# Optimization experiments

Measured on AMD Instinct MI355X. Metric: run time of the kernel, lower is better.

Reference implementation:

```python
import jax, jax.numpy as jnp
import numpy as np

M = 64          # SOM grid rows
N_GRID = 64     # SOM grid cols
DIM = 768       # SapBERT hidden size
COMPS = M * N_GRID
NBATCH = 8192   # number of embedded vectors per step


def setup_inputs() -> dict:
    key = jax.random.key(0)
    k1, k2 = jax.random.split(key)
    embedded = jax.random.normal(k1, (NBATCH, DIM), dtype=jnp.float32)
    contents = jax.random.normal(k2, (M, N_GRID, DIM), dtype=jnp.float32)
    # grid_dists: squared pairwise distances between grid coordinates (pdist2 in init_grid)
    x, y = np.meshgrid(range(M), range(N_GRID))
    g = np.stack([x, y]).reshape(2, -1).astype(np.float32)  # [2, comps]
    sq = (g ** 2).sum(0)
    gd = sq[:, None] + sq[None, :] - 2.0 * (g.T @ g)
    grid_dists = jnp.asarray(gd, dtype=jnp.float32)
    sigma = jnp.float32(max(M, N_GRID) / 2.0)
    return {"embedded": embedded, "contents": contents,
            "grid_dists": grid_dists, "sigma": sigma}


def reference(embedded, contents, grid_dists, sigma):
    comps = grid_dists.shape[0]
    dim = embedded.shape[1]
    flat_c = contents.reshape(comps, dim)
    # Gaussian neighborhood weights (compute_weight, weighted=True)
    weights = jnp.exp(-grid_dists / (2.0 * sigma ** 2))  # [comps, comps]
    # find_bmu: squared L2 dist + argmin (expanded form, same argmin as
    # the materialized N x comps x dim diff tensor in the original)
    dist = ((embedded ** 2).sum(-1, keepdims=True)
            + (flat_c ** 2).sum(-1)[None, :]
            - 2.0 * embedded @ flat_c.T)                 # [N, comps]
    min_idx = jnp.argmin(dist, axis=1)                   # [N]
    # scatter-accumulate counts and sums per codebook entry (index_add_)
    freq = jnp.zeros((comps,), embedded.dtype).at[min_idx].add(1.0)
    sums = jnp.zeros((comps, dim), embedded.dtype).at[min_idx].add(embedded)
    used = freq > 0
    avg = jnp.where(used[:, None], sums / jnp.maximum(freq, 1.0)[:, None], flat_c)
    # freq_weights[i,j] = weights[i,j] * freq[i]; update_num = sum_j fw[i,j]*avg[j,d]
    num = freq[:, None] * (weights @ avg)                # [comps, dim]
    denom = freq * weights.sum(axis=1)                   # [comps]
    update = num / jnp.where(used, denom, 1.0)[:, None]
    new_flat = jnp.where(used[:, None], update, flat_c)  # only update_denom!=0 rows
    new_contents = new_flat.reshape(contents.shape)
    delta = jnp.linalg.norm(new_contents - contents, axis=-1).sum()
    return delta, new_contents
```

## Files before the change

### kernel.cpp

```cpp
#include <hip/hip_runtime.h>

#define NB 8192
#define COMPS 4096
#define DIM 768

typedef _Float16 half8_t __attribute__((ext_vector_type(8)));
typedef float floatx4 __attribute__((ext_vector_type(4)));
typedef unsigned short ushort4_t __attribute__((ext_vector_type(4)));
typedef unsigned short ushort8_t __attribute__((ext_vector_type(8)));
typedef unsigned long long ullx2 __attribute__((ext_vector_type(2)));

typedef __attribute__((address_space(1))) const void* gas_ptr;
typedef __attribute__((address_space(3))) void* las_ptr;

__device__ __forceinline__ void gl_lds16(const _Float16* g, _Float16* l) {
  __builtin_amdgcn_global_load_lds((gas_ptr)(const void*)g, (las_ptr)(void*)l, 16, 0, 0);
}

__device__ __forceinline__ unsigned long long pack_min(float v, int col) {
  unsigned u = __float_as_uint(v);
  u = (u & 0x80000000u) ? ~u : (u | 0x80000000u);
  return ((unsigned long long)u << 32) | (unsigned)col;
}

#define PREP_GRID 13401
__global__ void k_prep(const float* __restrict__ e, const float* __restrict__ c,
                       const float* __restrict__ sigma,
                       _Float16* __restrict__ ehi, _Float16* __restrict__ elo,
                       _Float16* __restrict__ chi, _Float16* __restrict__ clo,
                       float* __restrict__ cnorm, float* __restrict__ E,
                       float* __restrict__ rE, float* __restrict__ sums,
                       float* __restrict__ freq, float* __restrict__ rowsq,
                       unsigned long long* __restrict__ packed,
                       unsigned int* __restrict__ done) {
  int bx = blockIdx.x, t = threadIdx.x;
  if (bx < 6144) {
    int id = bx * 256 + t;
    float4 v = ((const float4*)e)[id];
    ushort4_t h, l;
    float xs[4] = {v.x, v.y, v.z, v.w};
#pragma unroll
    for (int q = 0; q < 4; ++q) {
      _Float16 hh = (_Float16)xs[q];
      _Float16 ll = (_Float16)(xs[q] - (float)hh);
      h[q] = __builtin_bit_cast(unsigned short, hh);
      l[q] = __builtin_bit_cast(unsigned short, ll);
    }
    ((ushort4_t*)ehi)[id] = h;
    ((ushort4_t*)elo)[id] = l;
  } else if (bx < 10240) {
    int i = bx - 6144;
    float s = 0.f;
    if (t < 192) {
      float4 v = ((const float4*)c)[i * 192 + t];
      float xs[4] = {v.x, v.y, v.z, v.w};
      ushort4_t h, l;
#pragma unroll
      for (int q = 0; q < 4; ++q) {
        _Float16 hh = (_Float16)xs[q];
        _Float16 ll = (_Float16)(xs[q] - (float)hh);
        h[q] = __builtin_bit_cast(unsigned short, hh);
        l[q] = __builtin_bit_cast(unsigned short, ll);
        s = fmaf(xs[q], xs[q], s);
      }
      ((ushort4_t*)chi)[i * 192 + t] = h;
      ((ushort4_t*)clo)[i * 192 + t] = l;
    }
#pragma unroll
    for (int o = 32; o; o >>= 1) s += __shfl_down(s, o);
    __shared__ float red[3];
    if (t < 192 && (t & 63) == 0) red[t >> 6] = s;
    __syncthreads();
    if (t == 0) cnorm[i] = red[0] + red[1] + red[2];
  } else if (bx < 10304) {
    int i = bx - 10240;
    if (t < 64) {
      float sg = sigma[0];
      float inv = -1.0f / (2.0f * sg * sg);
      float d = (float)(i - t);
      float v = expf(d * d * inv);
      E[i * 64 + t] = v;
      float s = v;
#pragma unroll
      for (int o = 32; o; o >>= 1) s += __shfl_down(s, o);
      if (t == 0) rE[i] = s;
    }
  } else if (bx < 13376) {
    int id = (bx - 10304) * 256 + t;
    floatx4 z = {0.f, 0.f, 0.f, 0.f};
    ((floatx4*)sums)[id] = z;
  } else if (bx < 13392) {
    int id = (bx - 13376) * 256 + t;
    ullx2 f = {~0ULL, ~0ULL};
    ((ullx2*)packed)[id] = f;
  } else if (bx < 13396) {
    int id = (bx - 13392) * 256 + t;
    floatx4 z = {0.f, 0.f, 0.f, 0.f};
    ((floatx4*)freq)[id] = z;
  } else if (bx < 13400) {
    int id = (bx - 13396) * 256 + t;
    floatx4 z = {0.f, 0.f, 0.f, 0.f};
    ((floatx4*)rowsq)[id] = z;
  } else {
    if (t == 0) *done = 0u;
  }
}

__launch_bounds__(256)
__global__ void k_gemm1(const _Float16* __restrict__ ehi, const _Float16* __restrict__ elo,
                        const _Float16* __restrict__ chi, const _Float16* __restrict__ clo,
                        const float* __restrict__ cnorm,
                        unsigned long long* __restrict__ packed) {
  __shared__ _Float16 Ah[128 * 64], Al[128 * 64], Bh[128 * 64], Bl[128 * 64];
  int tid = threadIdx.x;
  int lane = tid & 63, w = tid >> 6;
  int wr = w >> 1, wc = w & 1;
  int g = lane >> 4, rl = lane & 15;
  int i0 = blockIdx.x * 128, j0 = blockIdx.y * 128;

  int lr = lane >> 3, lc = lane & 7;
  int cch = lc ^ lr;
  const _Float16* gsrc;
  _Float16* dbuf;
  if (w == 0)      { gsrc = ehi + (size_t)i0 * DIM; dbuf = Ah; }
  else if (w == 1) { gsrc = elo + (size_t)i0 * DIM; dbuf = Al; }
  else if (w == 2) { gsrc = chi + (size_t)j0 * DIM; dbuf = Bh; }
  else             { gsrc = clo + (size_t)j0 * DIM; dbuf = Bl; }
  gsrc += (size_t)lr * DIM + cch * 8;
  _Float16* dst = dbuf + lane * 8;

  floatx4 acc[4][4] = {};

  for (int kt = 0; kt < DIM; kt += 64) {
    __syncthreads();
#pragma unroll
    for (int q = 0; q < 16; ++q)
      gl_lds16(gsrc + kt + (size_t)(q * 8) * DIM, dst + q * 512);
    __syncthreads();

#pragma unroll
    for (int s = 0; s < 2; ++s) {
      half8_t ah[4], al[4];
#pragma unroll
      for (int m = 0; m < 4; ++m) {
        int r = wr * 64 + m * 16 + rl;
        int p = (s * 4 + g) ^ (rl & 7);
        ah[m] = *(half8_t*)&Ah[r * 64 + p * 8];
        al[m] = *(half8_t*)&Al[r * 64 + p * 8];
      }
#pragma unroll
      for (int n = 0; n < 4; ++n) {
        int r = wc * 64 + n * 16 + rl;
        int p = (s * 4 + g) ^ (rl & 7);
        half8_t bh = *(half8_t*)&Bh[r * 64 + p * 8];
        half8_t bl = *(half8_t*)&Bl[r * 64 + p * 8];
#pragma unroll
        for (int m = 0; m < 4; ++m) {
          acc[m][n] = __builtin_amdgcn_mfma_f32_16x16x32_f16(ah[m], bh, acc[m][n], 0, 0, 0);
          acc[m][n] = __builtin_amdgcn_mfma_f32_16x16x32_f16(ah[m], bl, acc[m][n], 0, 0, 0);
          acc[m][n] = __builtin_amdgcn_mfma_f32_16x16x32_f16(al[m], bh, acc[m][n], 0, 0, 0);
        }
      }
    }
  }

  float cn[4];
#pragma unroll
  for (int n = 0; n < 4; ++n) cn[n] = cnorm[j0 + wc * 64 + n * 16 + rl];

#pragma unroll
  for (int m = 0; m < 4; ++m) {
#pragma unroll
    for (int j = 0; j < 4; ++j) {
      int row = i0 + wr * 64 + m * 16 + g * 4 + j;
      float best = 3.0e38f;
      int bcol = 0;
#pragma unroll
      for (int n = 0; n < 4; ++n) {
        float d = fmaf(-2.0f, acc[m][n][j], cn[n]);
        int col = j0 + wc * 64 + n * 16 + rl;
        if (d < best) { best = d; bcol = col; }
      }
      unsigned long long pk = pack_min(best, bcol);
#pragma unroll
      for (int o = 1; o < 16; o <<= 1) {
        unsigned long long other = __shfl_xor(pk, o);
        if (other < pk) pk = other;
      }
      if (rl == 0) atomicMin(&packed[row], pk);
    }
  }
}

__global__ void k_scatter(const float* __restrict__ e,
                          const unsigned long long* __restrict__ packed,
                          float* __restrict__ freq, float* __restrict__ sums) {
  int i = blockIdx.x, t = threadIdx.x;
  int idx = (int)(packed[i] & 0xffffffffULL);
  if (t == 0) unsafeAtomicAdd(&freq[idx], 1.0f);
#pragma unroll
  for (int r = 0; r < 3; ++r) {
    int d = t + 256 * r;
    unsafeAtomicAdd(&sums[(size_t)idx * DIM + d], e[(size_t)i * DIM + d]);
  }
}

__global__ void k_t1(const float* __restrict__ sums, const float* __restrict__ freq,
                     const float* __restrict__ cont, const float* __restrict__ E,
                     float* __restrict__ T1) {
  __shared__ float S[64 * 128];
  __shared__ float Esh[64 * 64];
  int a = blockIdx.x, db = blockIdx.y, t = threadIdx.x;
#pragma unroll
  for (int it = 0; it < 8; ++it) {
    int id = t + 256 * it;
    int row = id >> 5, c4 = id & 31;
    int comp = a * 64 + row;
    float f = freq[comp];
    size_t o = (size_t)comp * 192 + db * 32 + c4;
    floatx4 v;
    if (f > 0.f) {
      floatx4 sv = ((const floatx4*)sums)[o];
      float inv = 1.0f / f;
      v = sv * inv;
    } else v = ((const floatx4*)cont)[o];
    ((floatx4*)S)[id] = v;
  }
#pragma unroll
  for (int it = 0; it < 4; ++it) {
    int id = t + 256 * it;
    ((floatx4*)Esh)[id] = ((const floatx4*)E)[id];
  }
  __syncthreads();

  int d4 = t & 31, b0 = (t >> 5) * 8;
  floatx4 acc[8] = {};
  for (int bp = 0; bp < 64; ++bp) {
    floatx4 sv = ((floatx4*)S)[bp * 32 + d4];
#pragma unroll
    for (int b = 0; b < 8; ++b)
      acc[b] += Esh[(b0 + b) * 64 + bp] * sv;
  }
#pragma unroll
  for (int b = 0; b < 8; ++b)
    ((floatx4*)T1)[(size_t)(a * 64 + b0 + b) * 192 + db * 32 + d4] = acc[b];
}

__global__ void k_wnum(const float* __restrict__ T1, const float* __restrict__ E,
                       const float* __restrict__ rE, const float* __restrict__ freq,
                       const float* __restrict__ cont, float* __restrict__ out,
                       float* __restrict__ rowsq, unsigned int* __restrict__ done) {
  __shared__ float S[64 * 128];
  __shared__ float Esh[64 * 64];
  int b = blockIdx.x, db = blockIdx.y, t = threadIdx.x;
#pragma unroll
  for (int it = 0; it < 8; ++it) {
    int id = t + 256 * it;
    int ap = id >> 5, c4 = id & 31;
    ((floatx4*)S)[id] = ((const floatx4*)T1)[(size_t)(ap * 64 + b) * 192 + db * 32 + c4];
  }
#pragma unroll
  for (int it = 0; it < 4; ++it) {
    int id = t + 256 * it;
    ((floatx4*)Esh)[id] = ((const floatx4*)E)[id];
  }
  __syncthreads();

  int d4 = t & 31, a0 = (t >> 5) * 8;
  floatx4 acc[8] = {};
  for (int ap = 0; ap < 64; ++ap) {
    floatx4 tv = ((floatx4*)S)[ap * 32 + d4];
#pragma unroll
    for (int a = 0; a < 8; ++a)
      acc[a] += Esh[(a0 + a) * 64 + ap] * tv;
  }

  float rb = rE[b];
  float sq[8];
#pragma unroll
  for (int a = 0; a < 8; ++a) {
    int comp = (a0 + a) * 64 + b;
    bool used = freq[comp] > 0.f;
    floatx4 cv = ((const floatx4*)cont)[(size_t)comp * 192 + db * 32 + d4];
    floatx4 val;
    if (used) {
      float inv = 1.0f / (rE[a0 + a] * rb);
      val = acc[a] * inv;
    } else val = cv;
    size_t base = 1 + (size_t)comp * DIM + db * 128 + d4 * 4;
    out[base] = val[0]; out[base + 1] = val[1];
    out[base + 2] = val[2]; out[base + 3] = val[3];
    floatx4 df = val - cv;
    sq[a] = df[0] * df[0] + df[1] * df[1] + df[2] * df[2] + df[3] * df[3];
  }
#pragma unroll
  for (int a = 0; a < 8; ++a) {
#pragma unroll
    for (int o = 1; o < 32; o <<= 1) sq[a] += __shfl_xor(sq[a], o);
  }
  if (d4 == 0) {
#pragma unroll
    for (int a = 0; a < 8; ++a)
      unsafeAtomicAdd(&rowsq[(a0 + a) * 64 + b], sq[a]);
  }

  __shared__ unsigned int lastflag;
  __syncthreads();
  if (t == 0) {
    __threadfence();
    unsigned int old = atomicAdd(done, 1u);
    lastflag = (old == 64u * 6u - 1u) ? 1u : 0u;
  }
  __syncthreads();
  if (lastflag) {
    double s = 0.0;
    for (int c2 = t; c2 < COMPS; c2 += 256) {
      float r = __hip_atomic_load(&rowsq[c2], __ATOMIC_RELAXED,
                                  __HIP_MEMORY_SCOPE_AGENT);
      s += sqrt((double)r);
    }
#pragma unroll
    for (int o = 32; o; o >>= 1) s += __shfl_down(s, o);
    __shared__ double red[4];
    if ((t & 63) == 0) red[t >> 6] = s;
    __syncthreads();
    if (t == 0) out[0] = (float)(red[0] + red[1] + red[2] + red[3]);
  }
}

extern "C" void kernel_launch(void* const* d_in, const int* in_sizes, int n_in,
                              void* d_out, int out_size, void* d_ws, size_t ws_size,
                              hipStream_t stream) {
  const float* e = (const float*)d_in[0];
  const float* cont = (const float*)d_in[1];
  const float* sigma = (const float*)d_in[3];
  float* out = (float*)d_out;

  char* ws = (char*)d_ws;
  size_t off = 0;
  auto take = [&](size_t bytes) { char* p = ws + off; off += (bytes + 255) & ~(size_t)255; return p; };

  unsigned long long* packed = (unsigned long long*)take(NB * 8);
  float* freq  = (float*)take(COMPS * 4);
  float* rowsq = (float*)take(COMPS * 4);
  float* cnorm = (float*)take(COMPS * 4);
  float* E     = (float*)take(64 * 64 * 4);
  float* rE    = (float*)take(64 * 4);
  unsigned int* done = (unsigned int*)take(256);
  float* sums  = (float*)take((size_t)COMPS * DIM * 4);
  char* U = take((size_t)NB * DIM * 2 * 2 + (size_t)COMPS * DIM * 2 * 2);
  _Float16* ehi = (_Float16*)U;
  _Float16* elo = (_Float16*)(U + (size_t)NB * DIM * 2);
  _Float16* chi = (_Float16*)(U + (size_t)NB * DIM * 4);
  _Float16* clo = (_Float16*)(U + (size_t)NB * DIM * 4 + (size_t)COMPS * DIM * 2);
  float* T1 = (float*)(U + (size_t)NB * DIM * 4);

  k_prep<<<PREP_GRID, 256, 0, stream>>>(e, cont, sigma, ehi, elo, chi, clo,
                                        cnorm, E, rE, sums, freq, rowsq,
                                        packed, done);
  k_gemm1<<<dim3(NB / 128, COMPS / 128), 256, 0, stream>>>(ehi, elo, chi, clo, cnorm, packed);
  k_scatter<<<NB, 256, 0, stream>>>(e, packed, freq, sums);
  k_t1<<<dim3(64, 6), 256, 0, stream>>>(sums, freq, cont, E, T1);
  k_wnum<<<dim3(64, 6), 256, 0, stream>>>(T1, E, rE, freq, cont, out, rowsq, done);
}
```

Before: 345.6 us.

## Double-buffer GEMM LDS tiles and fuse tail kernels with grid barriers

The distance GEMM now uses a K-step of 32 and two LDS buffers, so the global-to-LDS loads for the next tile are issued while the current tile is being multiplied. This replaces the earlier single-buffered 64-wide tile that stalled on a full sync before each compute step, and it drops the XOR swizzle. The scatter, T1 and wnum kernels are merged into one persistent 384-block kernel separated by software grid barriers, which removes two kernel launches. The grid barriers rely on all 384 blocks being resident at once, and dropping the swizzle may cause LDS bank conflicts.

```diff
diff --git a/kernel.cpp b/kernel.cpp
--- a/kernel.cpp
+++ b/kernel.cpp
@@ -3,11 +3,11 @@
 #define NB 8192
 #define COMPS 4096
 #define DIM 768
+#define TAIL_BLOCKS 384
 
 typedef _Float16 half8_t __attribute__((ext_vector_type(8)));
 typedef float floatx4 __attribute__((ext_vector_type(4)));
 typedef unsigned short ushort4_t __attribute__((ext_vector_type(4)));
-typedef unsigned short ushort8_t __attribute__((ext_vector_type(8)));
 typedef unsigned long long ullx2 __attribute__((ext_vector_type(2)));
 
 typedef __attribute__((address_space(1))) const void* gas_ptr;
@@ -32,7 +32,7 @@
                        float* __restrict__ rE, float* __restrict__ sums,
                        float* __restrict__ freq, float* __restrict__ rowsq,
                        unsigned long long* __restrict__ packed,
-                       unsigned int* __restrict__ done) {
+                       unsigned int* __restrict__ tk) {
   int bx = blockIdx.x, t = threadIdx.x;
   if (bx < 6144) {
     int id = bx * 256 + t;
@@ -102,7 +102,7 @@
     floatx4 z = {0.f, 0.f, 0.f, 0.f};
     ((floatx4*)rowsq)[id] = z;
   } else {
-    if (t == 0) *done = 0u;
+    if (t < 64) tk[t] = 0u;
   }
 }
 
@@ -111,57 +111,65 @@
                         const _Float16* __restrict__ chi, const _Float16* __restrict__ clo,
                         const float* __restrict__ cnorm,
                         unsigned long long* __restrict__ packed) {
-  __shared__ _Float16 Ah[128 * 64], Al[128 * 64], Bh[128 * 64], Bl[128 * 64];
+  __shared__ _Float16 lds[2][4][128 * 32];
   int tid = threadIdx.x;
   int lane = tid & 63, w = tid >> 6;
   int wr = w >> 1, wc = w & 1;
   int g = lane >> 4, rl = lane & 15;
   int i0 = blockIdx.x * 128, j0 = blockIdx.y * 128;
 
-  int lr = lane >> 3, lc = lane & 7;
-  int cch = lc ^ lr;
+  int lr = lane >> 2, lc = lane & 3;
   const _Float16* gsrc;
-  _Float16* dbuf;
-  if (w == 0)      { gsrc = ehi + (size_t)i0 * DIM; dbuf = Ah; }
-  else if (w == 1) { gsrc = elo + (size_t)i0 * DIM; dbuf = Al; }
-  else if (w == 2) { gsrc = chi + (size_t)j0 * DIM; dbuf = Bh; }
-  else             { gsrc = clo + (size_t)j0 * DIM; dbuf = Bl; }
-  gsrc += (size_t)lr * DIM + cch * 8;
-  _Float16* dst = dbuf + lane * 8;
+  if (w == 0)      gsrc = ehi + (size_t)i0 * DIM;
+  else if (w == 1) gsrc = elo + (size_t)i0 * DIM;
+  else if (w == 2) gsrc = chi + (size_t)j0 * DIM;
+  else             gsrc = clo + (size_t)j0 * DIM;
+  gsrc += (size_t)lr * DIM + lc * 8;
 
   floatx4 acc[4][4] = {};
 
-  for (int kt = 0; kt < DIM; kt += 64) {
-    __syncthreads();
-#pragma unroll
-    for (int q = 0; q < 16; ++q)
-      gl_lds16(gsrc + kt + (size_t)(q * 8) * DIM, dst + q * 512);
-    __syncthreads();
-
-#pragma unroll
-    for (int s = 0; s < 2; ++s) {
-      half8_t ah[4], al[4];
+  {
+    _Float16* dst = &lds[0][w][0] + lane * 8;
+#pragma unroll
+    for (int q = 0; q < 8; ++q)
+      gl_lds16(gsrc + (size_t)(q * 16) * DIM, dst + q * 512);
+  }
+  __syncthreads();
+
+  const int NT = DIM / 32;
+  for (int t = 0; t < NT; ++t) {
+    int cur = t & 1;
+    if (t + 1 < NT) {
+      const _Float16* gs = gsrc + (t + 1) * 32;
+      _Float16* dst = &lds[cur ^ 1][w][0] + lane * 8;
+#pragma unroll
+      for (int q = 0; q < 8; ++q)
+        gl_lds16(gs + (size_t)(q * 16) * DIM, dst + q * 512);
+    }
+    const _Float16* Ah = lds[cur][0];
+    const _Float16* Al = lds[cur][1];
+    const _Float16* Bh = lds[cur][2];
+    const _Float16* Bl = lds[cur][3];
+    half8_t ah[4], al[4];
+#pragma unroll
+    for (int m = 0; m < 4; ++m) {
+      int off = (wr * 64 + m * 16 + rl) * 32 + g * 8;
+      ah[m] = *(const half8_t*)&Ah[off];
+      al[m] = *(const half8_t*)&Al[off];
+    }
+#pragma unroll
+    for (int n = 0; n < 4; ++n) {
+      int off = (wc * 64 + n * 16 + rl) * 32 + g * 8;
+      half8_t bh = *(const half8_t*)&Bh[off];
+      half8_t bl = *(const half8_t*)&Bl[off];
 #pragma unroll
       for (int m = 0; m < 4; ++m) {
-        int r = wr * 64 + m * 16 + rl;
-        int p = (s * 4 + g) ^ (rl & 7);
-        ah[m] = *(half8_t*)&Ah[r * 64 + p * 8];
-        al[m] = *(half8_t*)&Al[r * 64 + p * 8];
-      }
-#pragma unroll
-      for (int n = 0; n < 4; ++n) {
-        int r = wc * 64 + n * 16 + rl;
-        int p = (s * 4 + g) ^ (rl & 7);
-        half8_t bh = *(half8_t*)&Bh[r * 64 + p * 8];
-        half8_t bl = *(half8_t*)&Bl[r * 64 + p * 8];
-#pragma unroll
-        for (int m = 0; m < 4; ++m) {
-          acc[m][n] = __builtin_amdgcn_mfma_f32_16x16x32_f16(ah[m], bh, acc[m][n], 0, 0, 0);
-          acc[m][n] = __builtin_amdgcn_mfma_f32_16x16x32_f16(ah[m], bl, acc[m][n], 0, 0, 0);
-          acc[m][n] = __builtin_amdgcn_mfma_f32_16x16x32_f16(al[m], bh, acc[m][n], 0, 0, 0);
-        }
-      }
-    }
+        acc[m][n] = __builtin_amdgcn_mfma_f32_16x16x32_f16(ah[m], bh, acc[m][n], 0, 0, 0);
+        acc[m][n] = __builtin_amdgcn_mfma_f32_16x16x32_f16(ah[m], bl, acc[m][n], 0, 0, 0);
+        acc[m][n] = __builtin_amdgcn_mfma_f32_16x16x32_f16(al[m], bh, acc[m][n], 0, 0, 0);
+      }
+    }
+    __syncthreads();
   }
 
   float cn[4];
@@ -192,139 +200,152 @@
   }
 }
 
-__global__ void k_scatter(const float* __restrict__ e,
-                          const unsigned long long* __restrict__ packed,
-                          float* __restrict__ freq, float* __restrict__ sums) {
-  int i = blockIdx.x, t = threadIdx.x;
-  int idx = (int)(packed[i] & 0xffffffffULL);
-  if (t == 0) unsafeAtomicAdd(&freq[idx], 1.0f);
-#pragma unroll
-  for (int r = 0; r < 3; ++r) {
-    int d = t + 256 * r;
-    unsafeAtomicAdd(&sums[(size_t)idx * DIM + d], e[(size_t)i * DIM + d]);
-  }
-}
-
-__global__ void k_t1(const float* __restrict__ sums, const float* __restrict__ freq,
-                     const float* __restrict__ cont, const float* __restrict__ E,
-                     float* __restrict__ T1) {
+__device__ __forceinline__ void gbar(unsigned int* tk) {
+  __syncthreads();
+  if (threadIdx.x == 0) {
+    __hip_atomic_fetch_add(tk, 1u, __ATOMIC_RELEASE, __HIP_MEMORY_SCOPE_AGENT);
+    while (__hip_atomic_load(tk, __ATOMIC_ACQUIRE, __HIP_MEMORY_SCOPE_AGENT)
+           < (unsigned)TAIL_BLOCKS) {
+      __builtin_amdgcn_s_sleep(8);
+    }
+  }
+  __syncthreads();
+}
+
+__launch_bounds__(256, 2)
+__global__ void k_tail(const float* __restrict__ e,
+                       const unsigned long long* __restrict__ packed,
+                       const float* __restrict__ cont, const float* __restrict__ E,
+                       const float* __restrict__ rE,
+                       float* __restrict__ freq, float* __restrict__ sums,
+                       float* __restrict__ T1, float* __restrict__ rowsq,
+                       float* __restrict__ out, unsigned int* __restrict__ tk) {
   __shared__ float S[64 * 128];
   __shared__ float Esh[64 * 64];
-  int a = blockIdx.x, db = blockIdx.y, t = threadIdx.x;
-#pragma unroll
-  for (int it = 0; it < 8; ++it) {
-    int id = t + 256 * it;
-    int row = id >> 5, c4 = id & 31;
-    int comp = a * 64 + row;
-    float f = freq[comp];
-    size_t o = (size_t)comp * 192 + db * 32 + c4;
-    floatx4 v;
-    if (f > 0.f) {
-      floatx4 sv = ((const floatx4*)sums)[o];
-      float inv = 1.0f / f;
-      v = sv * inv;
-    } else v = ((const floatx4*)cont)[o];
-    ((floatx4*)S)[id] = v;
+  int bid = blockIdx.x, t = threadIdx.x;
+
+  for (int i = bid; i < NB; i += TAIL_BLOCKS) {
+    int idx = (int)(packed[i] & 0xffffffffULL);
+    if (t == 0) unsafeAtomicAdd(&freq[idx], 1.0f);
+#pragma unroll
+    for (int r = 0; r < 3; ++r) {
+      int d = t + 256 * r;
+      unsafeAtomicAdd(&sums[(size_t)idx * DIM + d], e[(size_t)i * DIM + d]);
+    }
   }
 #pragma unroll
   for (int it = 0; it < 4; ++it) {
     int id = t + 256 * it;
     ((floatx4*)Esh)[id] = ((const floatx4*)E)[id];
   }
-  __syncthreads();
-
-  int d4 = t & 31, b0 = (t >> 5) * 8;
-  floatx4 acc[8] = {};
-  for (int bp = 0; bp < 64; ++bp) {
-    floatx4 sv = ((floatx4*)S)[bp * 32 + d4];
-#pragma unroll
-    for (int b = 0; b < 8; ++b)
-      acc[b] += Esh[(b0 + b) * 64 + bp] * sv;
-  }
-#pragma unroll
-  for (int b = 0; b < 8; ++b)
-    ((floatx4*)T1)[(size_t)(a * 64 + b0 + b) * 192 + db * 32 + d4] = acc[b];
-}
-
-__global__ void k_wnum(const float* __restrict__ T1, const float* __restrict__ E,
-                       const float* __restrict__ rE, const float* __restrict__ freq,
-                       const float* __restrict__ cont, float* __restrict__ out,
-                       float* __restrict__ rowsq, unsigned int* __restrict__ done) {
-  __shared__ float S[64 * 128];
-  __shared__ float Esh[64 * 64];
-  int b = blockIdx.x, db = blockIdx.y, t = threadIdx.x;
-#pragma unroll
-  for (int it = 0; it < 8; ++it) {
-    int id = t + 256 * it;
-    int ap = id >> 5, c4 = id & 31;
-    ((floatx4*)S)[id] = ((const floatx4*)T1)[(size_t)(ap * 64 + b) * 192 + db * 32 + c4];
-  }
-#pragma unroll
-  for (int it = 0; it < 4; ++it) {
-    int id = t + 256 * it;
-    ((floatx4*)Esh)[id] = ((const floatx4*)E)[id];
-  }
-  __syncthreads();
-
-  int d4 = t & 31, a0 = (t >> 5) * 8;
-  floatx4 acc[8] = {};
-  for (int ap = 0; ap < 64; ++ap) {
-    floatx4 tv = ((floatx4*)S)[ap * 32 + d4];
-#pragma unroll
-    for (int a = 0; a < 8; ++a)
-      acc[a] += Esh[(a0 + a) * 64 + ap] * tv;
-  }
-
-  float rb = rE[b];
-  float sq[8];
-#pragma unroll
-  for (int a = 0; a < 8; ++a) {
-    int comp = (a0 + a) * 64 + b;
-    bool used = freq[comp] > 0.f;
-    floatx4 cv = ((const floatx4*)cont)[(size_t)comp * 192 + db * 32 + d4];
-    floatx4 val;
-    if (used) {
-      float inv = 1.0f / (rE[a0 + a] * rb);
-      val = acc[a] * inv;
-    } else val = cv;
-    size_t base = 1 + (size_t)comp * DIM + db * 128 + d4 * 4;
-    out[base] = val[0]; out[base + 1] = val[1];
-    out[base + 2] = val[2]; out[base + 3] = val[3];
-    floatx4 df = val - cv;
-    sq[a] = df[0] * df[0] + df[1] * df[1] + df[2] * df[2] + df[3] * df[3];
-  }
-#pragma unroll
-  for (int a = 0; a < 8; ++a) {
-#pragma unroll
-    for (int o = 1; o < 32; o <<= 1) sq[a] += __shfl_xor(sq[a], o);
-  }
-  if (d4 == 0) {
-#pragma unroll
-    for (int a = 0; a < 8; ++a)
-      unsafeAtomicAdd(&rowsq[(a0 + a) * 64 + b], sq[a]);
-  }
-
-  __shared__ unsigned int lastflag;
-  __syncthreads();
-  if (t == 0) {
-    __threadfence();
-    unsigned int old = atomicAdd(done, 1u);
-    lastflag = (old == 64u * 6u - 1u) ? 1u : 0u;
-  }
-  __syncthreads();
-  if (lastflag) {
-    double s = 0.0;
-    for (int c2 = t; c2 < COMPS; c2 += 256) {
-      float r = __hip_atomic_load(&rowsq[c2], __ATOMIC_RELAXED,
-                                  __HIP_MEMORY_SCOPE_AGENT);
-      s += sqrt((double)r);
-    }
-#pragma unroll
-    for (int o = 32; o; o >>= 1) s += __shfl_down(s, o);
-    __shared__ double red[4];
-    if ((t & 63) == 0) red[t >> 6] = s;
-    __syncthreads();
-    if (t == 0) out[0] = (float)(red[0] + red[1] + red[2] + red[3]);
+  gbar(&tk[0]);
+
+  {
+    int a = bid / 6, db = bid % 6;
+#pragma unroll
+    for (int it = 0; it < 8; ++it) {
+      int id = t + 256 * it;
+      int row = id >> 5, c4 = id & 31;
+      int comp = a * 64 + row;
+      float f = freq[comp];
+      size_t o = (size_t)comp * 192 + db * 32 + c4;
+      floatx4 v;
+      if (f > 0.f) {
+        floatx4 sv = ((const floatx4*)sums)[o];
+        v = sv * (1.0f / f);
+      } else v = ((const floatx4*)cont)[o];
+      ((floatx4*)S)[id] = v;
+    }
+    __syncthreads();
+
+    int d4 = t & 31, b0 = (t >> 5) * 8;
+    floatx4 acc[8] = {};
+    for (int bp = 0; bp < 64; ++bp) {
+      floatx4 sv = ((floatx4*)S)[bp * 32 + d4];
+#pragma unroll
+      for (int b = 0; b < 8; ++b)
+        acc[b] += Esh[(b0 + b) * 64 + bp] * sv;
+    }
+#pragma unroll
+    for (int b = 0; b < 8; ++b) {
+      size_t base = ((size_t)(a * 64 + b0 + b) * 192 + db * 32 + d4) * 4;
+#pragma unroll
+      for (int q = 0; q < 4; ++q)
+        __hip_atomic_store(&T1[base + q], acc[b][q], __ATOMIC_RELAXED,
+                           __HIP_MEMORY_SCOPE_AGENT);
+    }
+  }
+  gbar(&tk[1]);
+
+  {
+    int b = bid / 6, db = bid % 6;
+#pragma unroll
+    for (int it = 0; it < 8; ++it) {
+      int id = t + 256 * it;
+      int ap = id >> 5, c4 = id & 31;
+      ((floatx4*)S)[id] =
+          ((const floatx4*)T1)[(size_t)(ap * 64 + b) * 192 + db * 32 + c4];
+    }
+    __syncthreads();
+
+    int d4 = t & 31, a0 = (t >> 5) * 8;
+    floatx4 acc[8] = {};
+    for (int ap = 0; ap < 64; ++ap) {
+      floatx4 tv = ((floatx4*)S)[ap * 32 + d4];
+#pragma unroll
+      for (int a = 0; a < 8; ++a)
+        acc[a] += Esh[(a0 + a) * 64 + ap] * tv;
+    }
+
+    float rb = rE[b];
+    float sq[8];
+#pragma unroll
+    for (int a = 0; a < 8; ++a) {
+      int comp = (a0 + a) * 64 + b;
+      bool used = freq[comp] > 0.f;
+      floatx4 cv = ((const floatx4*)cont)[(size_t)comp * 192 + db * 32 + d4];
+      floatx4 val;
+      if (used) val = acc[a] * (1.0f / (rE[a0 + a] * rb));
+      else val = cv;
+      size_t base = 1 + (size_t)comp * DIM + db * 128 + d4 * 4;
+      out[base] = val[0]; out[base + 1] = val[1];
+      out[base + 2] = val[2]; out[base + 3] = val[3];
+      floatx4 df = val - cv;
+      sq[a] = df[0] * df[0] + df[1] * df[1] + df[2] * df[2] + df[3] * df[3];
+    }
+#pragma unroll
+    for (int a = 0; a < 8; ++a) {
+#pragma unroll
+      for (int o = 1; o < 32; o <<= 1) sq[a] += __shfl_xor(sq[a], o);
+    }
+    if (d4 == 0) {
+#pragma unroll
+      for (int a = 0; a < 8; ++a)
+        unsafeAtomicAdd(&rowsq[(a0 + a) * 64 + b], sq[a]);
+    }
+
+    __shared__ unsigned int lastflag;
+    __syncthreads();
+    if (t == 0) {
+      unsigned int old = __hip_atomic_fetch_add(&tk[2], 1u, __ATOMIC_ACQ_REL,
+                                                __HIP_MEMORY_SCOPE_AGENT);
+      lastflag = (old == (unsigned)TAIL_BLOCKS - 1u) ? 1u : 0u;
+    }
+    __syncthreads();
+    if (lastflag) {
+      double s = 0.0;
+      for (int c2 = t; c2 < COMPS; c2 += 256) {
+        float r = __hip_atomic_load(&rowsq[c2], __ATOMIC_RELAXED,
+                                    __HIP_MEMORY_SCOPE_AGENT);
+        s += sqrt((double)r);
+      }
+#pragma unroll
+      for (int o = 32; o; o >>= 1) s += __shfl_down(s, o);
+      __shared__ double red[4];
+      if ((t & 63) == 0) red[t >> 6] = s;
+      __syncthreads();
+      if (t == 0) out[0] = (float)(red[0] + red[1] + red[2] + red[3]);
+    }
   }
 }
 
@@ -346,7 +367,7 @@
   float* cnorm = (float*)take(COMPS * 4);
   float* E     = (float*)take(64 * 64 * 4);
   float* rE    = (float*)take(64 * 4);
-  unsigned int* done = (unsigned int*)take(256);
+  unsigned int* tk = (unsigned int*)take(256);
   float* sums  = (float*)take((size_t)COMPS * DIM * 4);
   char* U = take((size_t)NB * DIM * 2 * 2 + (size_t)COMPS * DIM * 2 * 2);
   _Float16* ehi = (_Float16*)U;
@@ -357,9 +378,8 @@
 
   k_prep<<<PREP_GRID, 256, 0, stream>>>(e, cont, sigma, ehi, elo, chi, clo,
                                         cnorm, E, rE, sums, freq, rowsq,
-                                        packed, done);
+                                        packed, tk);
   k_gemm1<<<dim3(NB / 128, COMPS / 128), 256, 0, stream>>>(ehi, elo, chi, clo, cnorm, packed);
-  k_scatter<<<NB, 256, 0, stream>>>(e, packed, freq, sums);
-  k_t1<<<dim3(64, 6), 256, 0, stream>>>(sums, freq, cont, E, T1);
-  k_wnum<<<dim3(64, 6), 256, 0, stream>>>(T1, E, rE, freq, cont, out, rowsq, done);
-}
+  k_tail<<<TAIL_BLOCKS, 256, 0, stream>>>(e, packed, cont, E, rE, freq, sums,
+                                          T1, rowsq, out, tk);
+}
```

Result: slower. 470.5 us (+36.2%).
